# Kernel tuning notes

Hardware: AMD Instinct MI355X
Metric: run time of the kernel (lower is better)

Reference implementation:

```python
import jax, jax.numpy as jnp
import numpy as np

K_TOP = 128
NORM_TYPE = 'l2'  # 'l2' | 'l1' | 'avg'

def _norm(x, norm_type):
    if norm_type == 'l2':
        return jnp.sum(jnp.square(x), axis=2)
    if norm_type == 'l1':
        return jnp.sum(jnp.abs(x), axis=2)
    return jnp.sum(x, axis=2)  # 'avg'

def setup_inputs() -> dict:
    key = jax.random.key(0)
    x = jax.random.normal(key, (64, 8192, 256), dtype=jnp.float32)
    return {"x": x}

def reference(x) -> jnp.ndarray:
    # x: [B, N, D]
    norms = _norm(x, NORM_TYPE)                      # [B, N]
    _, idx = jax.lax.top_k(norms, K_TOP)             # [B, k], descending-norm order
    # gather the k selected embedding rows per batch element -> [B, k, D]
    return jnp.take_along_axis(x, idx[:, :, None], axis=1)
```

## Files before the change

### kernel.cpp

```cpp
#include <hip/hip_runtime.h>

constexpr int B = 64;
constexpr int N = 8192;
constexpr int D = 256;
constexpr int K = 128;
constexpr int CHUNKS = 32;
constexpr int RPC = N / CHUNKS;
constexpr int NCAND = CHUNKS * K;

typedef unsigned long long ull;

__global__ __launch_bounds__(256) void norm_select_kernel(const float* __restrict__ x,
                                                          ull* __restrict__ cand) {
    __shared__ ull skeys[RPC];
    const int bid   = blockIdx.x;
    const int batch = bid >> 5;
    const int chunk = bid & (CHUNKS - 1);
    const int tid   = threadIdx.x;
    const int w     = tid >> 6;
    const int lane  = tid & 63;
    const size_t rowbase = (size_t)batch * N + (size_t)chunk * RPC;
    const float* wbase = x + (rowbase + (size_t)w * 64) * D;

    for (int it = 0; it < 64; it += 8) {
        float4 v[8];
        #pragma unroll
        for (int u = 0; u < 8; ++u)
            v[u] = reinterpret_cast<const float4*>(wbase + (size_t)(it + u) * D)[lane];
        #pragma unroll
        for (int u = 0; u < 8; ++u) {
            float s = v[u].x * v[u].x + v[u].y * v[u].y
                    + v[u].z * v[u].z + v[u].w * v[u].w;
            #pragma unroll
            for (int off = 32; off > 0; off >>= 1)
                s += __shfl_xor(s, off, 64);
            if (lane == 0) {
                const int lrow = w * 64 + it + u;
                const int grow = chunk * RPC + lrow;
                skeys[lrow] = ((ull)__float_as_uint(s) << 32)
                            | (unsigned int)(N - 1 - grow);
            }
        }
    }
    __syncthreads();

    const ull mine = skeys[tid];
    int rank = 0;
    for (int j = 0; j < RPC; ++j)
        rank += (skeys[j] > mine) ? 1 : 0;
    if (rank < K)
        cand[(size_t)bid * K + rank] = mine;
}

__global__ __launch_bounds__(1024) void topk_gather_kernel(const ull* __restrict__ cand_in,
                                                           const float* __restrict__ x,
                                                           float* __restrict__ out) {
    __shared__ ull keys[NCAND];
    __shared__ unsigned int hist[256];
    __shared__ unsigned int seg[32];
    __shared__ ull s_prefix;
    __shared__ unsigned int s_krem;
    __shared__ int s_done;
    __shared__ unsigned int s_cnt;
    __shared__ ull sel[K];
    __shared__ int sorted_src[K];

    const int b    = blockIdx.x;
    const int tid  = threadIdx.x;
    const int lane = tid & 63;

    for (int i = tid; i < NCAND; i += 1024)
        keys[i] = cand_in[(size_t)b * NCAND + i];
    if (tid == 0) { s_prefix = 0ull; s_krem = K; s_done = 0; s_cnt = 0u; }
    __syncthreads();

    for (int p = 7; p >= 0; --p) {
        if (s_done) break;
        const int shift = p * 8;
        const ull          prefix = s_prefix;
        const unsigned int krem   = s_krem;
        if (tid < 256) hist[tid] = 0u;
        __syncthreads();

        if (p == 7) {
            for (int i = tid; i < NCAND; i += 1024) {
                const unsigned int d = (unsigned int)(keys[i] >> 56);
                ull rem = __ballot(true);
                while (rem) {
                    const int leader = __ffsll(rem) - 1;
                    const unsigned int dl = __shfl(d, leader, 64);
                    const ull grp = __ballot(d == dl);
                    if (lane == leader) atomicAdd(&hist[dl], (unsigned int)__popcll(grp));
                    rem &= ~grp;
                }
            }
        } else {
            for (int i = tid; i < NCAND; i += 1024) {
                const ull key = keys[i];
                if ((key >> (shift + 8)) == (prefix >> (shift + 8)))
                    atomicAdd(&hist[(unsigned int)(key >> shift) & 255u], 1u);
            }
        }
        __syncthreads();

        if (tid < 32) {
            unsigned int s = 0;
            #pragma unroll
            for (int d2 = 0; d2 < 8; ++d2) s += hist[tid * 8 + d2];
            seg[tid] = s;
        }
        __syncthreads();

        if (tid < 256) {
            unsigned int cnt_gt = 0;
            const int hiSeg = (tid >> 3) + 1;
            for (int s2 = hiSeg; s2 < 32; ++s2) cnt_gt += seg[s2];
            for (int d2 = tid + 1; d2 < hiSeg * 8; ++d2) cnt_gt += hist[d2];
            const unsigned int h = hist[tid];
            if (cnt_gt < krem && krem <= cnt_gt + h) {
                s_prefix = prefix | ((ull)tid << shift);
                s_krem   = krem - cnt_gt;
                if (h == krem - cnt_gt) s_done = 1;
            }
        }
        __syncthreads();
    }

    const ull T = s_prefix;
    for (int i = tid; i < NCAND; i += 1024) {
        const ull key = keys[i];
        if (key >= T) {
            const unsigned int pos = atomicAdd(&s_cnt, 1u);
            sel[pos] = key;
        }
    }
    __syncthreads();

    if (tid < K) {
        const ull key = sel[tid];
        int rank = 0;
        for (int j = 0; j < K; ++j) rank += (sel[j] > key) ? 1 : 0;
        sorted_src[rank] = N - 1 - (int)(key & 0xFFFFFFFFu);
    }
    __syncthreads();

    for (int r = tid >> 6; r < K; r += 16) {
        const int src = sorted_src[r];
        const float4 v = reinterpret_cast<const float4*>(x + ((size_t)b * N + src) * D)[lane];
        reinterpret_cast<float4*>(out + ((size_t)b * K + r) * D)[lane] = v;
    }
}

extern "C" void kernel_launch(void* const* d_in, const int* in_sizes, int n_in,
                              void* d_out, int out_size, void* d_ws, size_t ws_size,
                              hipStream_t stream) {
    const float* x = (const float*)d_in[0];
    float* out = (float*)d_out;
    ull* cand = (ull*)d_ws;

    norm_select_kernel<<<B * CHUNKS, 256, 0, stream>>>(x, cand);
    topk_gather_kernel<<<B, 1024, 0, stream>>>(cand, x, out);
}
```

Before: 126.8 us.

## Replace per-row wave shuffle reductions with shared-memory transpose reduction

Row norms were previously reduced with a 6-step cross-lane shuffle per row. Now each lane writes its partial sum into a padded shared tile, indexed by bit-reversed lane so the later adds follow the same order as the shuffle tree. One wave of 64 threads then sums each row serially in a fixed tree. This removes the shuffles but adds two block barriers per tile and a serial 64-element reduction on a quarter of the threads, and it cuts the number of loads in flight per wave from 8 to 4.

```diff
diff --git a/kernel.cpp b/kernel.cpp
--- a/kernel.cpp
+++ b/kernel.cpp
@@ -7,11 +7,18 @@
 constexpr int CHUNKS = 32;
 constexpr int RPC = N / CHUNKS;
 constexpr int NCAND = CHUNKS * K;
+constexpr int TILE = 64;
 
 typedef unsigned long long ull;
 
+__device__ __forceinline__ int bitrev6(int l) {
+    return ((l & 1) << 5) | ((l & 2) << 3) | ((l & 4) << 1)
+         | ((l & 8) >> 1) | ((l & 16) >> 3) | ((l & 32) >> 5);
+}
+
 __global__ __launch_bounds__(256) void norm_select_kernel(const float* __restrict__ x,
                                                           ull* __restrict__ cand) {
+    __shared__ float part[TILE][65];
     __shared__ ull skeys[RPC];
     const int bid   = blockIdx.x;
     const int batch = bid >> 5;
@@ -19,30 +26,43 @@
     const int tid   = threadIdx.x;
     const int w     = tid >> 6;
     const int lane  = tid & 63;
+    const int brl   = bitrev6(lane);
     const size_t rowbase = (size_t)batch * N + (size_t)chunk * RPC;
-    const float* wbase = x + (rowbase + (size_t)w * 64) * D;
 
-    for (int it = 0; it < 64; it += 8) {
-        float4 v[8];
+    for (int tile = 0; tile < 4; ++tile) {
+        const int r0 = w * 16;
+        const float* wbase = x + (rowbase + (size_t)(tile * TILE + r0)) * D;
         #pragma unroll
-        for (int u = 0; u < 8; ++u)
-            v[u] = reinterpret_cast<const float4*>(wbase + (size_t)(it + u) * D)[lane];
-        #pragma unroll
-        for (int u = 0; u < 8; ++u) {
-            float s = v[u].x * v[u].x + v[u].y * v[u].y
-                    + v[u].z * v[u].z + v[u].w * v[u].w;
+        for (int it0 = 0; it0 < 16; it0 += 4) {
+            float4 v[4];
             #pragma unroll
-            for (int off = 32; off > 0; off >>= 1)
-                s += __shfl_xor(s, off, 64);
-            if (lane == 0) {
-                const int lrow = w * 64 + it + u;
-                const int grow = chunk * RPC + lrow;
-                skeys[lrow] = ((ull)__float_as_uint(s) << 32)
-                            | (unsigned int)(N - 1 - grow);
+            for (int u = 0; u < 4; ++u)
+                v[u] = reinterpret_cast<const float4*>(wbase + (size_t)(it0 + u) * D)[lane];
+            #pragma unroll
+            for (int u = 0; u < 4; ++u)
+                part[r0 + it0 + u][brl] = v[u].x * v[u].x + v[u].y * v[u].y
+                                        + v[u].z * v[u].z + v[u].w * v[u].w;
+        }
+        __syncthreads();
+
+        if (tid < TILE) {
+            float q[8];
+            float g[8];
+            #pragma unroll
+            for (int grp = 0; grp < 8; ++grp) {
+                #pragma unroll
+                for (int j = 0; j < 8; ++j) q[j] = part[tid][grp * 8 + j];
+                g[grp] = ((q[0] + q[1]) + (q[2] + q[3]))
+                       + ((q[4] + q[5]) + (q[6] + q[7]));
             }
+            const float s = ((g[0] + g[1]) + (g[2] + g[3]))
+                          + ((g[4] + g[5]) + (g[6] + g[7]));
+            const int grow = chunk * RPC + tile * TILE + tid;
+            skeys[tile * TILE + tid] = ((ull)__float_as_uint(s) << 32)
+                                     | (unsigned int)(N - 1 - grow);
         }
+        __syncthreads();
     }
-    __syncthreads();
 
     const ull mine = skeys[tid];
     int rank = 0;
```

After: 116.4 us. -8.2%, faster.
